# Optimization experiments

Hardware: AMD Instinct MI355X
Metric: run time of the kernel (lower is better)

The kernel has to match this reference:

```python
import jax, jax.numpy as jnp
import numpy as np

B, C, T, H, F, KS = 8, 512, 1024, 8, 2048, 3
K = C // H            # head channels = 64
ROPE_D = K // 2       # RoPE rotates half the head channels = 32
EPS = 1e-4


def setup_inputs() -> dict:
    key = jax.random.key(0)
    ks = jax.random.split(key, 12)
    s = 1.0 / np.sqrt(C)
    sf = 1.0 / np.sqrt(F)
    return {
        "x": jax.random.normal(ks[0], (B, C, T), jnp.float32),
        "x_mask": jnp.ones((B, 1, T), jnp.float32),
        "attn_mask": jnp.ones((B, 1, T, T), jnp.float32),
        "wq": jax.random.normal(ks[1], (C, C), jnp.float32) * s,
        "bq": jnp.zeros((C,), jnp.float32),
        "wk": jax.random.normal(ks[2], (C, C), jnp.float32) * s,
        "bk": jnp.zeros((C,), jnp.float32),
        "wv": jax.random.normal(ks[3], (C, C), jnp.float32) * s,
        "bv": jnp.zeros((C,), jnp.float32),
        "wo": jax.random.normal(ks[4], (C, C), jnp.float32) * s,
        "bo": jnp.zeros((C,), jnp.float32),
        "w1": jax.random.normal(ks[5], (F, C, KS), jnp.float32) * s,
        "b1": jnp.zeros((F,), jnp.float32),
        "w2": jax.random.normal(ks[6], (C, F, KS), jnp.float32) * sf,
        "b2": jnp.zeros((C,), jnp.float32),
        "g1": jnp.ones((C,), jnp.float32),
        "be1": jnp.zeros((C,), jnp.float32),
        "g2": jnp.ones((C,), jnp.float32),
        "be2": jnp.zeros((C,), jnp.float32),
    }


def _rope(x):
    # x: (B, H, T, K); rotate first ROPE_D channels, pass the rest through.
    t = x.shape[2]
    theta = 1.0 / (10000.0 ** (jnp.arange(0, ROPE_D, 2, dtype=jnp.float32) / ROPE_D))
    idx = jnp.arange(t, dtype=jnp.float32)[:, None] * theta[None, :]  # (T, d/2)
    idx2 = jnp.concatenate([idx, idx], axis=-1)                       # (T, d)
    cos, sin = jnp.cos(idx2), jnp.sin(idx2)                           # broadcast over B,H
    xr, xp = x[..., :ROPE_D], x[..., ROPE_D:]
    h = ROPE_D // 2
    neg = jnp.concatenate([-xr[..., h:], xr[..., :h]], axis=-1)
    return jnp.concatenate([xr * cos + neg * sin, xp], axis=-1)


def _ln(x, gamma, beta):
    # channel-wise LayerNorm over dim 1 of (B, C, T), eps=1e-4
    mean = jnp.mean(x, axis=1, keepdims=True)
    var = jnp.mean((x - mean) ** 2, axis=1, keepdims=True)
    xn = (x - mean) * jax.lax.rsqrt(var + EPS)
    return xn * gamma[None, :, None] + beta[None, :, None]


def _conv1d(x, w, b):
    # x: (B, Cin, T), w: (Cout, Cin, KS), 'same' padding (KS//2)
    y = jax.lax.conv_general_dilated(
        x, w, window_strides=(1,), padding=[(KS // 2, KS // 2)],
        dimension_numbers=("NCH", "OIH", "NCH"))
    return y + b[None, :, None]


def _forward(x, x_mask, attn_mask, wq, bq, wk, bk, wv, bv, wo, bo,
             w1, b1, w2, b2, g1, be1, g2, be2):
    x = x * x_mask
    # 1x1 conv projections == channel matmuls
    q = jnp.einsum("oc,bct->bot", wq, x) + bq[None, :, None]
    k = jnp.einsum("oc,bct->bot", wk, x) + bk[None, :, None]
    v = jnp.einsum("oc,bct->bot", wv, x) + bv[None, :, None]
    # (B, C, T) -> (B, H, T, K)
    def heads(a):
        return a.reshape(B, H, K, T).transpose(0, 1, 3, 2)
    q, k, v = heads(q), heads(k), heads(v)
    q = _rope(q)
    k = _rope(k)
    scores = jnp.einsum("bhtk,bhsk->bhts", q, k) / jnp.sqrt(jnp.float32(K))
    scores = jnp.where(attn_mask == 0, jnp.float32(-10000.0), scores)
    p = jax.nn.softmax(scores, axis=-1)
    o = jnp.einsum("bhts,bhsk->bhtk", p, v)              # (B,H,T,K)
    o = o.transpose(0, 1, 3, 2).reshape(B, C, T)
    y = jnp.einsum("oc,bct->bot", wo, o) + bo[None, :, None]
    x = _ln(x + y, g1, be1)
    # conv FFN
    h1 = jax.nn.relu(_conv1d(x * x_mask, w1, b1))
    y = _conv1d(h1 * x_mask, w2, b2) * x_mask
    x = _ln(x + y, g2, be2)
    return x


def reference(x, x_mask, attn_mask, wq, bq, wk, bk, wv, bv, wo, bo,
              w1, b1, w2, b2, g1, be1, g2, be2):
    return _forward(x, x_mask, attn_mask, wq, bq, wk, bk, wv, bv, wo, bo,
                    w1, b1, w2, b2, g1, be1, g2, be2)
```

## Files before the change

### kernel.cpp

```cpp
#include <hip/hip_runtime.h>

typedef unsigned short u16;
typedef __attribute__((ext_vector_type(4))) float floatx4;
typedef __attribute__((ext_vector_type(8))) __bf16 bf16x8;
typedef __attribute__((ext_vector_type(4))) unsigned short ushort4v;
typedef __attribute__((ext_vector_type(8))) unsigned short ushort8v;

#define DI __device__ __forceinline__


DI u16 f2bf(float f) {
  union { float f; unsigned u; } v; v.f = f;
  unsigned r = v.u + 0x7fffu + ((v.u >> 16) & 1u);
  return (u16)(r >> 16);
}
DI float bf2f(u16 h) {
  union { unsigned u; float f; } v; v.u = ((unsigned)h) << 16;
  return v.f;
}

#define GLDS(g, l) __builtin_amdgcn_global_load_lds( \
    (const __attribute__((address_space(1))) unsigned int*)(g), \
    (__attribute__((address_space(3))) unsigned int*)(l), 16, 0, 0)

__global__ __launch_bounds__(256) void k_fattn(
    const u16* __restrict__ qb, const u16* __restrict__ kb,
    const u16* __restrict__ vb, const unsigned* __restrict__ mb,
    u16* __restrict__ oT)
{
  __shared__ __align__(16) u16 Ps[4][32 * 64];
  const int tid  = threadIdx.x;
  const int wave = tid >> 6, lane = tid & 63;
  const int lr = lane & 15, kg = lane >> 4;
  const int qt = blockIdx.x, bh = blockIdx.y;
  const int bb = bh >> 3, hh = bh & 7;
  const int wq0 = qt * 128 + wave * 32;
  const float L2E = 1.44269504f;

  const u16* Qp = qb + (size_t)bh * 65536;
  const u16* Kp = kb + (size_t)bh * 65536;
  const u16* Vp = vb + (size_t)bh * 65536;
  u16* Pw = &Ps[wave][0];

  bf16x8 qf[2][2];
#pragma unroll
  for (int i = 0; i < 2; ++i)
#pragma unroll
    for (int h = 0; h < 2; ++h)
      qf[i][h] = *(const bf16x8*)&Qp[(wq0 + i * 16 + lr) * 64 + h * 32 + kg * 8];

  float m_b[2] = {-3.0e38f, -3.0e38f};
  float l_b[2] = {0.f, 0.f};
  floatx4 o_acc[2][4];
#pragma unroll
  for (int i = 0; i < 2; ++i)
#pragma unroll
    for (int j = 0; j < 4; ++j) o_acc[i][j] = (floatx4){0.f, 0.f, 0.f, 0.f};

  for (int s0 = 0; s0 < 1024; s0 += 64) {
    floatx4 sT[4][2];
#pragma unroll
    for (int a = 0; a < 4; ++a) {
      bf16x8 kf[2];
#pragma unroll
      for (int h = 0; h < 2; ++h)
        kf[h] = *(const bf16x8*)&Kp[(s0 + a * 16 + lr) * 64 + h * 32 + kg * 8];
      sT[a][0] = (floatx4){0.f, 0.f, 0.f, 0.f};
      sT[a][1] = (floatx4){0.f, 0.f, 0.f, 0.f};
#pragma unroll
      for (int b = 0; b < 2; ++b)
#pragma unroll
        for (int h = 0; h < 2; ++h)
          sT[a][b] = __builtin_amdgcn_mfma_f32_16x16x32_bf16(kf[h], qf[b][h], sT[a][b], 0, 0, 0);
    }
    float corr[2];
#pragma unroll
    for (int b = 0; b < 2; ++b) {
      const size_t rw = ((size_t)bb << 15) + ((size_t)(wq0 + b * 16 + lr) << 5) + (s0 >> 5);
      const unsigned w0 = mb[rw], w1 = mb[rw + 1];
      float mx = -3.0e38f;
#pragma unroll
      for (int a = 0; a < 4; ++a)
#pragma unroll
        for (int r = 0; r < 4; ++r) {
          const int sl = a * 16 + kg * 4 + r;
          float sv = sT[a][b][r] * 0.125f;
          const unsigned wsel = (sl & 32) ? w1 : w0;
          if (!((wsel >> (sl & 31)) & 1u)) sv = -10000.f;
          sT[a][b][r] = sv;
          mx = fmaxf(mx, sv);
        }
      mx = fmaxf(mx, __shfl_xor(mx, 16));
      mx = fmaxf(mx, __shfl_xor(mx, 32));
      const float mn = fmaxf(m_b[b], mx);
      corr[b] = exp2f((m_b[b] - mn) * L2E);
      m_b[b] = mn;
      float sum = 0.f;
#pragma unroll
      for (int a = 0; a < 4; ++a)
#pragma unroll
        for (int r = 0; r < 4; ++r) {
          const float p = exp2f((sT[a][b][r] - mn) * L2E);
          sT[a][b][r] = p;
          sum += p;
        }
      sum += __shfl_xor(sum, 16);
      sum += __shfl_xor(sum, 32);
      l_b[b] = l_b[b] * corr[b] + sum;
#pragma unroll
      for (int a = 0; a < 4; ++a)
#pragma unroll
        for (int r = 0; r < 4; ++r) {
          const int sl = a * 16 + kg * 4 + r;
          __bf16 hv = (__bf16)sT[a][b][r];
          Pw[(b * 16 + lr) * 64 + (sl ^ ((lr & 7) << 3))] = *(u16*)&hv;
        }
    }
#pragma unroll
    for (int i = 0; i < 2; ++i)
#pragma unroll
      for (int r = 0; r < 4; ++r) {
        const float cv = __shfl(corr[i], kg * 4 + r);
#pragma unroll
        for (int jd = 0; jd < 4; ++jd) o_acc[i][jd][r] *= cv;
      }
    asm volatile("s_waitcnt lgkmcnt(0)" ::: "memory");
    __builtin_amdgcn_sched_barrier(0);
    bf16x8 pa[2][2];
#pragma unroll
    for (int i = 0; i < 2; ++i)
#pragma unroll
      for (int h = 0; h < 2; ++h)
        pa[i][h] = *(const bf16x8*)&Pw[(i * 16 + lr) * 64 + (((h * 4 + kg) ^ (lr & 7)) << 3)];
#pragma unroll
    for (int jd = 0; jd < 4; ++jd) {
      bf16x8 vf[2];
#pragma unroll
      for (int h = 0; h < 2; ++h)
        vf[h] = *(const bf16x8*)&Vp[(jd * 16 + lr) * 1024 + s0 + h * 32 + kg * 8];
#pragma unroll
      for (int i = 0; i < 2; ++i)
#pragma unroll
        for (int h = 0; h < 2; ++h)
          o_acc[i][jd] = __builtin_amdgcn_mfma_f32_16x16x32_bf16(pa[i][h], vf[h], o_acc[i][jd], 0, 0, 0);
    }
  }
  float linv[2][4];
#pragma unroll
  for (int i = 0; i < 2; ++i)
#pragma unroll
    for (int r = 0; r < 4; ++r) linv[i][r] = 1.f / __shfl(l_b[i], kg * 4 + r);
#pragma unroll
  for (int i = 0; i < 2; ++i)
#pragma unroll
    for (int jd = 0; jd < 4; ++jd)
#pragma unroll
      for (int r = 0; r < 4; ++r) {
        const int t = wq0 + i * 16 + kg * 4 + r;
        const int c = hh * 64 + jd * 16 + lr;
        oT[((size_t)bb * 1024 + t) * 512 + c] = f2bf(o_acc[i][jd][r] * linv[i][r]);
      }
}

template<int MODE, int BN, int TAPK>
__global__ __launch_bounds__(256) void k_cgemm(
    const u16* __restrict__ A, int lda,
    const u16* __restrict__ Bsrc, int ldb,
    int K,
    u16* __restrict__ o0, u16* __restrict__ o1, u16* __restrict__ o2,
    const float* __restrict__ bias,
    const float* __restrict__ ctab, const float* __restrict__ stab,
    const float* __restrict__ msk)
{
  constexpr int BM = 128;
  constexpr int FN = BN / 32;
  __shared__ __align__(16) u16 As[2 * BM * 32];
  __shared__ __align__(16) u16 Bs[2 * BN * 32];

  const int tid  = threadIdx.x;
  const int wave = tid >> 6, lane = tid & 63;
  const int wm = wave >> 1, wn = wave & 1;
  const int lr = lane & 15, kg = lane >> 4;

  const int nwg = gridDim.x * gridDim.y;
  const int h0  = blockIdx.y * gridDim.x + blockIdx.x;
  const int cpx = nwg >> 3;
  const int tl  = (h0 & 7) * cpx + (h0 >> 3);
  const int bx  = tl % gridDim.x;
  const int by  = tl / gridDim.x;

  const int m0 = bx * BM, n0 = by * BN;
  const int koff = blockIdx.z * K;

  floatx4 acc[4][FN];
#pragma unroll
  for (int i = 0; i < 4; ++i)
#pragma unroll
    for (int j = 0; j < FN; ++j) acc[i][j] = (floatx4){0.f, 0.f, 0.f, 0.f};

  for (int k0 = 0; k0 < K; k0 += 64) {
#pragma unroll
    for (int h = 0; h < 2; ++h) {
      const int kglob = koff + k0 + h * 32;
#pragma unroll
      for (int ch = 0; ch < BM / 64; ++ch) {
        int idx = ch * 256 + tid;
        int row = idx >> 2, kk = (idx & 3) << 3;
        GLDS(A + (size_t)(m0 + row) * lda + (kglob + kk),
             &As[h * BM * 32 + idx * 8]);
      }
#pragma unroll
      for (int ch = 0; ch < BN / 64; ++ch) {
        int idx = ch * 256 + tid;
        int row = idx >> 2, kk = (idx & 3) << 3;
        const int bt = n0 + row;
        const u16* src;
        if constexpr (TAPK == 0) {
          src = Bsrc + (size_t)bt * ldb + (kglob + kk);
        } else {
          const int tap = kglob / TAPK, off2 = kglob - tap * TAPK;
          const int b = bt >> 10, t = bt & 1023;
          src = Bsrc + ((size_t)(b * 1026 + t + tap)) * TAPK + off2 + kk;
        }
        GLDS(src, &Bs[h * BN * 32 + idx * 8]);
      }
    }
    __syncthreads();
    bf16x8 af[2][4], bfr[2][FN];
#pragma unroll
    for (int h = 0; h < 2; ++h) {
#pragma unroll
      for (int i = 0; i < 4; ++i)
        af[h][i] = *(const bf16x8*)&As[(h * BM + wm * 64 + i * 16 + lr) * 32 + kg * 8];
#pragma unroll
      for (int j = 0; j < FN; ++j)
        bfr[h][j] = *(const bf16x8*)&Bs[(h * BN + wn * (BN / 2) + j * 16 + lr) * 32 + kg * 8];
    }
#pragma unroll
    for (int h = 0; h < 2; ++h)
#pragma unroll
      for (int i = 0; i < 4; ++i)
#pragma unroll
        for (int j = 0; j < FN; ++j)
          acc[i][j] = __builtin_amdgcn_mfma_f32_16x16x32_bf16(af[h][i], bfr[h][j], acc[i][j], 0, 0, 0);
    __syncthreads();
  }

  const int wrow0 = m0 + wm * 64;
  const int col0  = n0 + wn * (BN / 2);

  if constexpr (MODE == 0) {
    float v[4][FN][4];
#pragma unroll
    for (int i = 0; i < 4; ++i)
#pragma unroll
      for (int j = 0; j < FN; ++j)
#pragma unroll
        for (int r = 0; r < 4; ++r)
          v[i][j][r] = acc[i][j][r] + bias[wrow0 + i * 16 + kg * 4 + r];
    const int sec = wrow0 >> 9;
    const int hh  = (wrow0 & 511) >> 6;
    if (sec < 2) {
#pragma unroll
      for (int j = 0; j < FN; ++j) {
        const int t = (col0 + j * 16 + lr) & 1023;
#pragma unroll
        for (int r = 0; r < 4; ++r) {
          const int a = kg * 4 + r;
          const float cv = ctab[t * 16 + a], sv = stab[t * 16 + a];
          const float a0 = v[0][j][r], a1 = v[1][j][r];
          v[0][j][r] = a0 * cv - a1 * sv;
          v[1][j][r] = a1 * cv + a0 * sv;
        }
      }
      u16* dst = (sec == 0) ? o0 : o1;
#pragma unroll
      for (int i = 0; i < 4; ++i)
#pragma unroll
        for (int j = 0; j < FN; ++j) {
          const int bt = col0 + j * 16 + lr;
          const int b = bt >> 10, t = bt & 1023;
          ushort4v pk;
#pragma unroll
          for (int r = 0; r < 4; ++r) pk[r] = f2bf(v[i][j][r]);
          *(ushort4v*)&dst[(((size_t)b * 8 + hh) * 1024 + t) * 64 + i * 16 + kg * 4] = pk;
        }
    } else {
#pragma unroll
      for (int i = 0; i < 4; ++i)
#pragma unroll
        for (int j = 0; j < FN; ++j) {
          const int bt = col0 + j * 16 + lr;
          const int b = bt >> 10, t = bt & 1023;
#pragma unroll
          for (int r = 0; r < 4; ++r) {
            const int dk = i * 16 + kg * 4 + r;
            o2[(((size_t)b * 8 + hh) * 64 + dk) * 1024 + t] = f2bf(v[i][j][r]);
          }
        }
    }
  } else if constexpr (MODE == 3) {
#pragma unroll
    for (int i = 0; i < 4; ++i)
#pragma unroll
      for (int j = 0; j < FN; ++j) {
        const int bt = col0 + j * 16 + lr;
        const int c0 = wrow0 + i * 16 + kg * 4;
        ushort4v pk;
#pragma unroll
        for (int r = 0; r < 4; ++r) pk[r] = f2bf(acc[i][j][r] + bias[c0 + r]);
        *(ushort4v*)&o0[(size_t)bt * 512 + c0] = pk;
      }
  } else if constexpr (MODE == 4) {
#pragma unroll
    for (int i = 0; i < 4; ++i) {
      const int r0 = wrow0 + i * 16 + kg * 4;
#pragma unroll
      for (int j = 0; j < FN; ++j) {
        const int bt = col0 + j * 16 + lr;
        const int b = bt >> 10, t = bt & 1023;
        const float mv = msk[(size_t)b * 1024 + t];
        ushort4v pk;
#pragma unroll
        for (int r = 0; r < 4; ++r)
          pk[r] = f2bf(fmaxf(acc[i][j][r] + bias[r0 + r], 0.f) * mv);
        *(ushort4v*)&o0[((size_t)(b * 1026 + t + 1)) * 2048 + r0] = pk;
      }
    }
  } else {
    u16* dst = (blockIdx.z == 0) ? o0 : o1;
#pragma unroll
    for (int i = 0; i < 4; ++i)
#pragma unroll
      for (int j = 0; j < FN; ++j) {
        const int bt = col0 + j * 16 + lr;
        const int b = bt >> 10, t = bt & 1023;
        const int c0 = wrow0 + i * 16 + kg * 4;
        const float mv = msk[(size_t)b * 1024 + t];
        ushort4v pk;
#pragma unroll
        for (int r = 0; r < 4; ++r) {
          const float bv = (blockIdx.z == 0) ? bias[c0 + r] : 0.f;
          pk[r] = f2bf((acc[i][j][r] + bv) * mv);
        }
        *(ushort4v*)&dst[(size_t)bt * 512 + c0] = pk;
      }
  }
}

__global__ __launch_bounds__(256) void k_cvt(const float* __restrict__ in, u16* __restrict__ out, int n) {
  int i = blockIdx.x * 256 + threadIdx.x;
  if (i < n) out[i] = f2bf(in[i]);
}

__global__ __launch_bounds__(256) void k_repack_w1(const float* __restrict__ in, u16* __restrict__ out) {
  int i = blockIdx.x * 256 + threadIdx.x;
  int f = i / 1536, rem = i % 1536;
  int kk = rem >> 9, c = rem & 511;
  out[i] = f2bf(in[f * 1536 + c * 3 + kk]);
}

__global__ __launch_bounds__(256) void k_repack_w2(const float* __restrict__ in, u16* __restrict__ out) {
  int i = blockIdx.x * 256 + threadIdx.x;
  int c = i / 6144, rem = i % 6144;
  int kk = rem >> 11, f = rem & 2047;
  out[i] = f2bf(in[c * 6144 + f * 3 + kk]);
}

__global__ __launch_bounds__(256) void k_bias_concat(const float* __restrict__ bq, const float* __restrict__ bk,
                                                     const float* __restrict__ bv, float* __restrict__ out) {
  int i = blockIdx.x * 256 + threadIdx.x;
  if (i < 512) out[i] = bq[i];
  else if (i < 1024) out[i] = bk[i - 512];
  else if (i < 1536) out[i] = bv[i - 1024];
}

__global__ __launch_bounds__(256) void k_rope_tables(float* __restrict__ ct, float* __restrict__ st) {
  int i = blockIdx.x * 256 + threadIdx.x;
  int t = i >> 4, a = i & 15;
  float theta = powf(10000.f, -(float)a / 16.f);
  float ang = (float)t * theta;
  ct[i] = cosf(ang);
  st[i] = sinf(ang);
}

__global__ __launch_bounds__(256) void k_maskpack(const float* __restrict__ am, unsigned* __restrict__ mb) {
  int i = blockIdx.x * 256 + threadIdx.x;
  const float* src = am + (size_t)i * 32;
  unsigned w = 0;
#pragma unroll
  for (int q = 0; q < 32; ++q) w |= (src[q] != 0.f) ? (1u << q) : 0u;
  mb[i] = w;
}

__global__ __launch_bounds__(256) void k_zrows(u16* __restrict__ p, int R) {
  const int b = blockIdx.x >> 1;
  const size_t row = (blockIdx.x & 1) ? 1025 : 0;
  u16* r = p + ((size_t)b * 1026 + row) * R;
  for (int i = threadIdx.x; i < R; i += 256) r[i] = 0;
}

__global__ __launch_bounds__(256) void k_tcvt(const float* __restrict__ in, u16* __restrict__ out,
                                              const float* __restrict__ msk, int R, int TT) {
  __shared__ u16 tile[64][65];
  const int b = blockIdx.z;
  const int r0 = blockIdx.x * 64, t0 = blockIdx.y * 64;
  const int tx = threadIdx.x & 63, ty = threadIdx.x >> 6;
  const float mv = msk ? msk[(size_t)b * TT + t0 + tx] : 1.f;
  const float* ib = in + (size_t)b * R * TT;
#pragma unroll
  for (int rr = ty; rr < 64; rr += 4)
    tile[rr][tx] = f2bf(ib[(size_t)(r0 + rr) * TT + t0 + tx] * mv);
  __syncthreads();
  u16* ob = out + (size_t)b * TT * R;
#pragma unroll
  for (int tt = ty; tt < 64; tt += 4)
    ob[(size_t)(t0 + tt) * R + r0 + tx] = tile[tx][tt];
}

__global__ __launch_bounds__(256) void k_ln1(
    const u16* __restrict__ xbT, const u16* __restrict__ y1T,
    const float* __restrict__ xm, const float* __restrict__ g,
    const float* __restrict__ be, u16* __restrict__ x2T, u16* __restrict__ x2p)
{
  const int lane = threadIdx.x & 63, wv = threadIdx.x >> 6;
  const int row = blockIdx.x * 4 + wv;
  const int b = row >> 10, t = row & 1023;
  const size_t base = (size_t)row * 512 + lane * 8;
  ushort8v ux = *(const ushort8v*)&xbT[base];
  ushort8v uy = *(const ushort8v*)&y1T[base];
  float v[8];
  float sum = 0.f, ss = 0.f;
#pragma unroll
  for (int q = 0; q < 8; ++q) {
    v[q] = bf2f(ux[q]) + bf2f(uy[q]);
    sum += v[q]; ss += v[q] * v[q];
  }
#pragma unroll
  for (int o = 32; o; o >>= 1) { sum += __shfl_xor(sum, o); ss += __shfl_xor(ss, o); }
  const float mean = sum * (1.f / 512.f);
  const float var  = ss * (1.f / 512.f) - mean * mean;
  const float rs   = rsqrtf(var + 1e-4f);
  const float m    = xm[(size_t)b * 1024 + t];
  ushort8v on, om;
#pragma unroll
  for (int q = 0; q < 8; ++q) {
    const int c = lane * 8 + q;
    const float nv = (v[q] - mean) * rs * g[c] + be[c];
    on[q] = f2bf(nv);
    om[q] = f2bf(nv * m);
  }
  *(ushort8v*)&x2T[base] = on;
  *(ushort8v*)&x2p[((size_t)(b * 1026 + t + 1)) * 512 + lane * 8] = om;
}

__global__ __launch_bounds__(256) void k_ln2_stats(
    const u16* __restrict__ x2T, const u16* __restrict__ y2a,
    const u16* __restrict__ y2b, float2* __restrict__ mr)
{
  const int lane = threadIdx.x & 63, wv = threadIdx.x >> 6;
  const int row = blockIdx.x * 4 + wv;
  const size_t base = (size_t)row * 512 + lane * 8;
  ushort8v u0 = *(const ushort8v*)&x2T[base];
  ushort8v u1 = *(const ushort8v*)&y2a[base];
  ushort8v u2 = *(const ushort8v*)&y2b[base];
  float sum = 0.f, ss = 0.f;
#pragma unroll
  for (int q = 0; q < 8; ++q) {
    const float v = bf2f(u0[q]) + bf2f(u1[q]) + bf2f(u2[q]);
    sum += v; ss += v * v;
  }
#pragma unroll
  for (int o = 32; o; o >>= 1) { sum += __shfl_xor(sum, o); ss += __shfl_xor(ss, o); }
  if (lane == 0) {
    const float mean = sum * (1.f / 512.f);
    const float var  = ss * (1.f / 512.f) - mean * mean;
    mr[row] = (float2){mean, rsqrtf(var + 1e-4f)};
  }
}

__global__ __launch_bounds__(256) void k_ln2_write(
    const u16* __restrict__ x2T, const u16* __restrict__ y2a,
    const u16* __restrict__ y2b, const float2* __restrict__ mr,
    const float* __restrict__ g, const float* __restrict__ be,
    float* __restrict__ out)
{
  __shared__ float tile[64][65];
  const int cc0 = blockIdx.x * 64, t0 = blockIdx.y * 64, b = blockIdx.z;
  const int tid = threadIdx.x;
  const int c4 = (tid & 15) * 4;
  const int tr = tid >> 4;
  float g4[4], b4[4];
#pragma unroll
  for (int q = 0; q < 4; ++q) { g4[q] = g[cc0 + c4 + q]; b4[q] = be[cc0 + c4 + q]; }
#pragma unroll
  for (int it = 0; it < 4; ++it) {
    const int tt = tr + it * 16;
    const int row = b * 1024 + t0 + tt;
    const size_t base = (size_t)row * 512 + cc0 + c4;
    ushort4v u0 = *(const ushort4v*)&x2T[base];
    ushort4v u1 = *(const ushort4v*)&y2a[base];
    ushort4v u2 = *(const ushort4v*)&y2b[base];
    const float2 s = mr[row];
#pragma unroll
    for (int q = 0; q < 4; ++q) {
      const float v = bf2f(u0[q]) + bf2f(u1[q]) + bf2f(u2[q]);
      tile[tt][c4 + q] = (v - s.x) * s.y * g4[q] + b4[q];
    }
  }
  __syncthreads();
  const int tx = tid & 63, cg = tid >> 6;
#pragma unroll
  for (int c = cg; c < 64; c += 4)
    out[((size_t)b * 512 + cc0 + c) * 1024 + t0 + tx] = tile[tx][c];
}

extern "C" void kernel_launch(void* const* d_in, const int* in_sizes, int n_in,
                              void* d_out, int out_size, void* d_ws, size_t ws_size,
                              hipStream_t stream) {
  (void)in_sizes; (void)n_in; (void)out_size; (void)ws_size;
  const float* x   = (const float*)d_in[0];
  const float* xm  = (const float*)d_in[1];
  const float* am  = (const float*)d_in[2];
  const float* wq  = (const float*)d_in[3];
  const float* bq  = (const float*)d_in[4];
  const float* wk  = (const float*)d_in[5];
  const float* bk  = (const float*)d_in[6];
  const float* wv  = (const float*)d_in[7];
  const float* bv  = (const float*)d_in[8];
  const float* wo  = (const float*)d_in[9];
  const float* bo  = (const float*)d_in[10];
  const float* w1  = (const float*)d_in[11];
  const float* b1  = (const float*)d_in[12];
  const float* w2  = (const float*)d_in[13];
  const float* b2  = (const float*)d_in[14];
  const float* g1  = (const float*)d_in[15];
  const float* be1 = (const float*)d_in[16];
  const float* g2  = (const float*)d_in[17];
  const float* be2 = (const float*)d_in[18];
  float* out = (float*)d_out;

  char* ws = (char*)d_ws;
  size_t off = 0;
  auto alloc = [&](size_t bytes) { char* p = ws + off; off += (bytes + 255) & ~(size_t)255; return p; };

  u16*   wqkv = (u16*)  alloc((size_t)1536 * 512 * 2);
  u16*   wob  = (u16*)  alloc((size_t)512 * 512 * 2);
  u16*   w1p  = (u16*)  alloc((size_t)2048 * 1536 * 2);
  u16*   w2p  = (u16*)  alloc((size_t)512 * 6144 * 2);
  float* bqkv = (float*)alloc(1536 * 4);
  float* ctab = (float*)alloc(1024 * 16 * 4);
  float* stab = (float*)alloc(1024 * 16 * 4);
  unsigned* mbits = (unsigned*)alloc((size_t)8 * 1024 * 32 * 4);
  float2* mr  = (float2*)alloc((size_t)8192 * 8);
  u16*   x2T  = (u16*)  alloc((size_t)8 * 1024 * 512 * 2);
  u16*   x2p  = (u16*)  alloc((size_t)8 * 1026 * 512 * 2);
  u16*   h1p  = (u16*)  alloc((size_t)8 * 1026 * 2048 * 2);
  u16*   y1T  = (u16*)  alloc((size_t)8 * 1024 * 512 * 2);
  u16*   xbT  = (u16*)  alloc((size_t)8 * 1024 * 512 * 2);
  u16*   oT   = (u16*)  alloc((size_t)8 * 1024 * 512 * 2);
  u16*   qkv3 = (u16*)  alloc((size_t)3 * 8 * 8 * 1024 * 64 * 2);

  u16* qb   = qkv3;
  u16* kb   = qkv3 + (size_t)8 * 8 * 1024 * 64;
  u16* vb   = kb   + (size_t)8 * 8 * 1024 * 64;
  u16* y2aT = y1T;
  u16* y2bT = oT;

  dim3 blk(256);

  k_cvt<<<dim3(1024), blk, 0, stream>>>(wq, wqkv, 512 * 512);
  k_cvt<<<dim3(1024), blk, 0, stream>>>(wk, wqkv + 512 * 512, 512 * 512);
  k_cvt<<<dim3(1024), blk, 0, stream>>>(wv, wqkv + 2 * 512 * 512, 512 * 512);
  k_cvt<<<dim3(1024), blk, 0, stream>>>(wo, wob, 512 * 512);
  k_repack_w1<<<dim3(12288), blk, 0, stream>>>(w1, w1p);
  k_repack_w2<<<dim3(12288), blk, 0, stream>>>(w2, w2p);
  k_bias_concat<<<dim3(6), blk, 0, stream>>>(bq, bk, bv, bqkv);
  k_rope_tables<<<dim3(64), blk, 0, stream>>>(ctab, stab);
  k_maskpack<<<dim3(1024), blk, 0, stream>>>(am, mbits);
  k_zrows<<<dim3(16), blk, 0, stream>>>(x2p, 512);
  k_zrows<<<dim3(16), blk, 0, stream>>>(h1p, 2048);

  k_tcvt<<<dim3(8, 16, 8), blk, 0, stream>>>(x, xbT, xm, 512, 1024);

  k_cgemm<0, 128, 0><<<dim3(12, 64), blk, 0, stream>>>(
      wqkv, 512, xbT, 512, 512, qb, kb, vb, bqkv, ctab, stab, nullptr);

  k_fattn<<<dim3(8, 64), blk, 0, stream>>>(qb, kb, vb, mbits, oT);

  k_cgemm<3, 64, 0><<<dim3(4, 128), blk, 0, stream>>>(
      wob, 512, oT, 512, 512, y1T, nullptr, nullptr, bo, nullptr, nullptr, nullptr);

  k_ln1<<<dim3(2048), blk, 0, stream>>>(xbT, y1T, xm, g1, be1, x2T, x2p);

  k_cgemm<4, 128, 512><<<dim3(16, 64), blk, 0, stream>>>(
      w1p, 1536, x2p, 0, 1536, h1p, nullptr, nullptr, b1, nullptr, nullptr, xm);
  k_cgemm<5, 64, 2048><<<dim3(4, 128, 2), blk, 0, stream>>>(
      w2p, 6144, h1p, 0, 3072, y2aT, y2bT, nullptr, b2, nullptr, nullptr, xm);

  k_ln2_stats<<<dim3(2048), blk, 0, stream>>>(x2T, y2aT, y2bT, mr);
  k_ln2_write<<<dim3(8, 16, 8), blk, 0, stream>>>(x2T, y2aT, y2bT, mr, g2, be2, out);
}
```

Before: 332.3 us.

## Double-buffer GEMM LDS tiles, XOR-swizzle LDS layout, shrink BN for QKV/FFN1

The shared GEMM kernel now ping-pongs two LDS buffers, so the global-to-LDS async loads for the next K-slice are issued before the MFMAs on the current slice. That removes one barrier per iteration and hides load latency. Row-dependent XOR swizzling of the 8-element column chunks is meant to cut LDS bank conflicts on the fragment reads. The QKV and first-conv GEMMs also switch from a 128 to a 64 column tile with twice the grid, which adds occupancy and offsets the doubled LDS footprint at the cost of less operand reuse per block.

```diff
diff --git a/kernel.cpp b/kernel.cpp
--- a/kernel.cpp
+++ b/kernel.cpp
@@ -174,8 +174,8 @@
 {
   constexpr int BM = 128;
   constexpr int FN = BN / 32;
-  __shared__ __align__(16) u16 As[2 * BM * 32];
-  __shared__ __align__(16) u16 Bs[2 * BN * 32];
+  __shared__ __align__(16) u16 As[2][2 * BM * 32];
+  __shared__ __align__(16) u16 Bs[2][2 * BN * 32];
 
   const int tid  = threadIdx.x;
   const int wave = tid >> 6, lane = tid & 63;
@@ -192,27 +192,23 @@
   const int m0 = bx * BM, n0 = by * BN;
   const int koff = blockIdx.z * K;
 
-  floatx4 acc[4][FN];
-#pragma unroll
-  for (int i = 0; i < 4; ++i)
-#pragma unroll
-    for (int j = 0; j < FN; ++j) acc[i][j] = (floatx4){0.f, 0.f, 0.f, 0.f};
-
-  for (int k0 = 0; k0 < K; k0 += 64) {
+  auto stage = [&](int buf, int kbase) {
 #pragma unroll
     for (int h = 0; h < 2; ++h) {
-      const int kglob = koff + k0 + h * 32;
+      const int kglob = kbase + h * 32;
 #pragma unroll
       for (int ch = 0; ch < BM / 64; ++ch) {
-        int idx = ch * 256 + tid;
-        int row = idx >> 2, kk = (idx & 3) << 3;
+        const int idx = ch * 256 + tid;
+        const int row = idx >> 2;
+        const int kk = (((idx & 3) ^ ((row >> 1) & 3)) << 3);
         GLDS(A + (size_t)(m0 + row) * lda + (kglob + kk),
-             &As[h * BM * 32 + idx * 8]);
+             &As[buf][h * BM * 32 + idx * 8]);
       }
 #pragma unroll
       for (int ch = 0; ch < BN / 64; ++ch) {
-        int idx = ch * 256 + tid;
-        int row = idx >> 2, kk = (idx & 3) << 3;
+        const int idx = ch * 256 + tid;
+        const int row = idx >> 2;
+        const int kk = (((idx & 3) ^ ((row >> 1) & 3)) << 3);
         const int bt = n0 + row;
         const u16* src;
         if constexpr (TAPK == 0) {
@@ -222,19 +218,33 @@
           const int b = bt >> 10, t = bt & 1023;
           src = Bsrc + ((size_t)(b * 1026 + t + tap)) * TAPK + off2 + kk;
         }
-        GLDS(src, &Bs[h * BN * 32 + idx * 8]);
-      }
-    }
-    __syncthreads();
+        GLDS(src, &Bs[buf][h * BN * 32 + idx * 8]);
+      }
+    }
+  };
+
+  floatx4 acc[4][FN];
+#pragma unroll
+  for (int i = 0; i < 4; ++i)
+#pragma unroll
+    for (int j = 0; j < FN; ++j) acc[i][j] = (floatx4){0.f, 0.f, 0.f, 0.f};
+
+  const int csw = (kg ^ ((lr >> 1) & 3)) * 8;
+
+  stage(0, koff);
+  __syncthreads();
+  int cur = 0;
+  for (int k0 = 0; k0 < K; k0 += 64) {
+    if (k0 + 64 < K) stage(cur ^ 1, koff + k0 + 64);
     bf16x8 af[2][4], bfr[2][FN];
 #pragma unroll
     for (int h = 0; h < 2; ++h) {
 #pragma unroll
       for (int i = 0; i < 4; ++i)
-        af[h][i] = *(const bf16x8*)&As[(h * BM + wm * 64 + i * 16 + lr) * 32 + kg * 8];
+        af[h][i] = *(const bf16x8*)&As[cur][(h * BM + wm * 64 + i * 16 + lr) * 32 + csw];
 #pragma unroll
       for (int j = 0; j < FN; ++j)
-        bfr[h][j] = *(const bf16x8*)&Bs[(h * BN + wn * (BN / 2) + j * 16 + lr) * 32 + kg * 8];
+        bfr[h][j] = *(const bf16x8*)&Bs[cur][(h * BN + wn * (BN / 2) + j * 16 + lr) * 32 + csw];
     }
 #pragma unroll
     for (int h = 0; h < 2; ++h)
@@ -244,6 +254,7 @@
         for (int j = 0; j < FN; ++j)
           acc[i][j] = __builtin_amdgcn_mfma_f32_16x16x32_bf16(af[h][i], bfr[h][j], acc[i][j], 0, 0, 0);
     __syncthreads();
+    cur ^= 1;
   }
 
   const int wrow0 = m0 + wm * 64;
@@ -583,7 +594,7 @@
 
   k_tcvt<<<dim3(8, 16, 8), blk, 0, stream>>>(x, xbT, xm, 512, 1024);
 
-  k_cgemm<0, 128, 0><<<dim3(12, 64), blk, 0, stream>>>(
+  k_cgemm<0, 64, 0><<<dim3(12, 128), blk, 0, stream>>>(
       wqkv, 512, xbT, 512, 512, qb, kb, vb, bqkv, ctab, stab, nullptr);
 
   k_fattn<<<dim3(8, 64), blk, 0, stream>>>(qb, kb, vb, mbits, oT);
@@ -593,7 +604,7 @@
 
   k_ln1<<<dim3(2048), blk, 0, stream>>>(xbT, y1T, xm, g1, be1, x2T, x2p);
 
-  k_cgemm<4, 128, 512><<<dim3(16, 64), blk, 0, stream>>>(
+  k_cgemm<4, 64, 512><<<dim3(16, 128), blk, 0, stream>>>(
       w1p, 1536, x2p, 0, 1536, h1p, nullptr, nullptr, b1, nullptr, nullptr, xm);
   k_cgemm<5, 64, 2048><<<dim3(4, 128, 2), blk, 0, stream>>>(
       w2p, 6144, h1p, 0, 3072, y2aT, y2bT, nullptr, b2, nullptr, nullptr, xm);
```

Measured after the change: 349.5 us. +5.2%, slower.

## Halve attention query tile per wave, prefetch K/V, swizzle GEMM LDS

Applied to the files above, without the earlier changes.

The flash-attention kernel now handles 16 query rows per wave instead of 32 and launches twice as many blocks. It also loads all K and V fragments before their MFMA loops and raises wave priority around those loops, aiming for more parallelism and better latency hiding. In exchange, each K/V load is reused by half as many queries, so global/L2 traffic roughly doubles. Separately, the GEMM kernel XOR-swizzles the 16-byte column chunks in LDS on both the write and read side to reduce bank conflicts.

```diff
diff --git a/kernel.cpp b/kernel.cpp
--- a/kernel.cpp
+++ b/kernel.cpp
@@ -28,13 +28,13 @@
     const u16* __restrict__ vb, const unsigned* __restrict__ mb,
     u16* __restrict__ oT)
 {
-  __shared__ __align__(16) u16 Ps[4][32 * 64];
+  __shared__ __align__(16) u16 Ps[4][16 * 64];
   const int tid  = threadIdx.x;
   const int wave = tid >> 6, lane = tid & 63;
   const int lr = lane & 15, kg = lane >> 4;
   const int qt = blockIdx.x, bh = blockIdx.y;
   const int bb = bh >> 3, hh = bh & 7;
-  const int wq0 = qt * 128 + wave * 32;
+  const int wq0 = qt * 64 + wave * 16;
   const float L2E = 1.44269504f;
 
   const u16* Qp = qb + (size_t)bh * 65536;
@@ -42,124 +42,110 @@
   const u16* Vp = vb + (size_t)bh * 65536;
   u16* Pw = &Ps[wave][0];
 
-  bf16x8 qf[2][2];
-#pragma unroll
-  for (int i = 0; i < 2; ++i)
-#pragma unroll
-    for (int h = 0; h < 2; ++h)
-      qf[i][h] = *(const bf16x8*)&Qp[(wq0 + i * 16 + lr) * 64 + h * 32 + kg * 8];
-
-  float m_b[2] = {-3.0e38f, -3.0e38f};
-  float l_b[2] = {0.f, 0.f};
-  floatx4 o_acc[2][4];
-#pragma unroll
-  for (int i = 0; i < 2; ++i)
-#pragma unroll
-    for (int j = 0; j < 4; ++j) o_acc[i][j] = (floatx4){0.f, 0.f, 0.f, 0.f};
+  bf16x8 qf[2];
+#pragma unroll
+  for (int h = 0; h < 2; ++h)
+    qf[h] = *(const bf16x8*)&Qp[(wq0 + lr) * 64 + h * 32 + kg * 8];
+
+  float m_b = -3.0e38f;
+  float l_b = 0.f;
+  floatx4 o_acc[4];
+#pragma unroll
+  for (int j = 0; j < 4; ++j) o_acc[j] = (floatx4){0.f, 0.f, 0.f, 0.f};
 
   for (int s0 = 0; s0 < 1024; s0 += 64) {
-    floatx4 sT[4][2];
+    floatx4 sT[4];
+    bf16x8 kf[4][2];
+#pragma unroll
+    for (int a = 0; a < 4; ++a)
+#pragma unroll
+      for (int h = 0; h < 2; ++h)
+        kf[a][h] = *(const bf16x8*)&Kp[(s0 + a * 16 + lr) * 64 + h * 32 + kg * 8];
+    __builtin_amdgcn_s_setprio(1);
 #pragma unroll
     for (int a = 0; a < 4; ++a) {
-      bf16x8 kf[2];
+      sT[a] = (floatx4){0.f, 0.f, 0.f, 0.f};
 #pragma unroll
       for (int h = 0; h < 2; ++h)
-        kf[h] = *(const bf16x8*)&Kp[(s0 + a * 16 + lr) * 64 + h * 32 + kg * 8];
-      sT[a][0] = (floatx4){0.f, 0.f, 0.f, 0.f};
-      sT[a][1] = (floatx4){0.f, 0.f, 0.f, 0.f};
-#pragma unroll
-      for (int b = 0; b < 2; ++b)
-#pragma unroll
-        for (int h = 0; h < 2; ++h)
-          sT[a][b] = __builtin_amdgcn_mfma_f32_16x16x32_bf16(kf[h], qf[b][h], sT[a][b], 0, 0, 0);
-    }
-    float corr[2];
-#pragma unroll
-    for (int b = 0; b < 2; ++b) {
-      const size_t rw = ((size_t)bb << 15) + ((size_t)(wq0 + b * 16 + lr) << 5) + (s0 >> 5);
-      const unsigned w0 = mb[rw], w1 = mb[rw + 1];
-      float mx = -3.0e38f;
-#pragma unroll
-      for (int a = 0; a < 4; ++a)
-#pragma unroll
-        for (int r = 0; r < 4; ++r) {
-          const int sl = a * 16 + kg * 4 + r;
-          float sv = sT[a][b][r] * 0.125f;
-          const unsigned wsel = (sl & 32) ? w1 : w0;
-          if (!((wsel >> (sl & 31)) & 1u)) sv = -10000.f;
-          sT[a][b][r] = sv;
-          mx = fmaxf(mx, sv);
-        }
-      mx = fmaxf(mx, __shfl_xor(mx, 16));
-      mx = fmaxf(mx, __shfl_xor(mx, 32));
-      const float mn = fmaxf(m_b[b], mx);
-      corr[b] = exp2f((m_b[b] - mn) * L2E);
-      m_b[b] = mn;
-      float sum = 0.f;
-#pragma unroll
-      for (int a = 0; a < 4; ++a)
-#pragma unroll
-        for (int r = 0; r < 4; ++r) {
-          const float p = exp2f((sT[a][b][r] - mn) * L2E);
-          sT[a][b][r] = p;
-          sum += p;
-        }
-      sum += __shfl_xor(sum, 16);
-      sum += __shfl_xor(sum, 32);
-      l_b[b] = l_b[b] * corr[b] + sum;
-#pragma unroll
-      for (int a = 0; a < 4; ++a)
-#pragma unroll
-        for (int r = 0; r < 4; ++r) {
-          const int sl = a * 16 + kg * 4 + r;
-          __bf16 hv = (__bf16)sT[a][b][r];
-          Pw[(b * 16 + lr) * 64 + (sl ^ ((lr & 7) << 3))] = *(u16*)&hv;
-        }
-    }
-#pragma unroll
-    for (int i = 0; i < 2; ++i)
+        sT[a] = __builtin_amdgcn_mfma_f32_16x16x32_bf16(kf[a][h], qf[h], sT[a], 0, 0, 0);
+    }
+    __builtin_amdgcn_s_setprio(0);
+    const size_t rw = ((size_t)bb << 15) + ((size_t)(wq0 + lr) << 5) + (s0 >> 5);
+    const unsigned w0 = mb[rw], w1 = mb[rw + 1];
+    float mx = -3.0e38f;
+#pragma unroll
+    for (int a = 0; a < 4; ++a)
 #pragma unroll
       for (int r = 0; r < 4; ++r) {
-        const float cv = __shfl(corr[i], kg * 4 + r);
-#pragma unroll
-        for (int jd = 0; jd < 4; ++jd) o_acc[i][jd][r] *= cv;
-      }
+        const int sl = a * 16 + kg * 4 + r;
+        float sv = sT[a][r] * 0.125f;
+        const unsigned wsel = (sl & 32) ? w1 : w0;
+        if (!((wsel >> (sl & 31)) & 1u)) sv = -10000.f;
+        sT[a][r] = sv;
+        mx = fmaxf(mx, sv);
+      }
+    mx = fmaxf(mx, __shfl_xor(mx, 16));
+    mx = fmaxf(mx, __shfl_xor(mx, 32));
+    const float mn = fmaxf(m_b, mx);
+    const float corr = exp2f((m_b - mn) * L2E);
+    m_b = mn;
+    float sum = 0.f;
+#pragma unroll
+    for (int a = 0; a < 4; ++a)
+#pragma unroll
+      for (int r = 0; r < 4; ++r) {
+        const float p = exp2f((sT[a][r] - mn) * L2E);
+        sT[a][r] = p;
+        sum += p;
+      }
+    sum += __shfl_xor(sum, 16);
+    sum += __shfl_xor(sum, 32);
+    l_b = l_b * corr + sum;
+#pragma unroll
+    for (int a = 0; a < 4; ++a)
+#pragma unroll
+      for (int r = 0; r < 4; ++r) {
+        const int sl = a * 16 + kg * 4 + r;
+        __bf16 hv = (__bf16)sT[a][r];
+        Pw[lr * 64 + (sl ^ ((lr & 7) << 3))] = *(u16*)&hv;
+      }
+#pragma unroll
+    for (int r = 0; r < 4; ++r) {
+      const float cv = __shfl(corr, kg * 4 + r);
+#pragma unroll
+      for (int jd = 0; jd < 4; ++jd) o_acc[jd][r] *= cv;
+    }
     asm volatile("s_waitcnt lgkmcnt(0)" ::: "memory");
     __builtin_amdgcn_sched_barrier(0);
-    bf16x8 pa[2][2];
-#pragma unroll
-    for (int i = 0; i < 2; ++i)
+    bf16x8 pa[2];
+#pragma unroll
+    for (int h = 0; h < 2; ++h)
+      pa[h] = *(const bf16x8*)&Pw[lr * 64 + (((h * 4 + kg) ^ (lr & 7)) << 3)];
+    bf16x8 vf[4][2];
+#pragma unroll
+    for (int jd = 0; jd < 4; ++jd)
 #pragma unroll
       for (int h = 0; h < 2; ++h)
-        pa[i][h] = *(const bf16x8*)&Pw[(i * 16 + lr) * 64 + (((h * 4 + kg) ^ (lr & 7)) << 3)];
-#pragma unroll
-    for (int jd = 0; jd < 4; ++jd) {
-      bf16x8 vf[2];
+        vf[jd][h] = *(const bf16x8*)&Vp[(jd * 16 + lr) * 1024 + s0 + h * 32 + kg * 8];
+    __builtin_amdgcn_s_setprio(1);
+#pragma unroll
+    for (int jd = 0; jd < 4; ++jd)
 #pragma unroll
       for (int h = 0; h < 2; ++h)
-        vf[h] = *(const bf16x8*)&Vp[(jd * 16 + lr) * 1024 + s0 + h * 32 + kg * 8];
-#pragma unroll
-      for (int i = 0; i < 2; ++i)
-#pragma unroll
-        for (int h = 0; h < 2; ++h)
-          o_acc[i][jd] = __builtin_amdgcn_mfma_f32_16x16x32_bf16(pa[i][h], vf[h], o_acc[i][jd], 0, 0, 0);
-    }
-  }
-  float linv[2][4];
-#pragma unroll
-  for (int i = 0; i < 2; ++i)
-#pragma unroll
-    for (int r = 0; r < 4; ++r) linv[i][r] = 1.f / __shfl(l_b[i], kg * 4 + r);
-#pragma unroll
-  for (int i = 0; i < 2; ++i)
-#pragma unroll
-    for (int jd = 0; jd < 4; ++jd)
-#pragma unroll
-      for (int r = 0; r < 4; ++r) {
-        const int t = wq0 + i * 16 + kg * 4 + r;
-        const int c = hh * 64 + jd * 16 + lr;
-        oT[((size_t)bb * 1024 + t) * 512 + c] = f2bf(o_acc[i][jd][r] * linv[i][r]);
-      }
+        o_acc[jd] = __builtin_amdgcn_mfma_f32_16x16x32_bf16(pa[h], vf[jd][h], o_acc[jd], 0, 0, 0);
+    __builtin_amdgcn_s_setprio(0);
+  }
+  float linv[4];
+#pragma unroll
+  for (int r = 0; r < 4; ++r) linv[r] = 1.f / __shfl(l_b, kg * 4 + r);
+#pragma unroll
+  for (int jd = 0; jd < 4; ++jd)
+#pragma unroll
+    for (int r = 0; r < 4; ++r) {
+      const int t = wq0 + kg * 4 + r;
+      const int c = hh * 64 + jd * 16 + lr;
+      oT[((size_t)bb * 1024 + t) * 512 + c] = f2bf(o_acc[jd][r] * linv[r]);
+    }
 }
 
 template<int MODE, int BN, int TAPK>
@@ -198,21 +184,25 @@
 #pragma unroll
     for (int j = 0; j < FN; ++j) acc[i][j] = (floatx4){0.f, 0.f, 0.f, 0.f};
 
+  const int csw = (kg ^ ((lr >> 1) & 3)) * 8;
+
   for (int k0 = 0; k0 < K; k0 += 64) {
 #pragma unroll
     for (int h = 0; h < 2; ++h) {
       const int kglob = koff + k0 + h * 32;
 #pragma unroll
       for (int ch = 0; ch < BM / 64; ++ch) {
-        int idx = ch * 256 + tid;
-        int row = idx >> 2, kk = (idx & 3) << 3;
+        const int idx = ch * 256 + tid;
+        const int row = idx >> 2;
+        const int kk = (((idx & 3) ^ ((row >> 1) & 3)) << 3);
         GLDS(A + (size_t)(m0 + row) * lda + (kglob + kk),
              &As[h * BM * 32 + idx * 8]);
       }
 #pragma unroll
       for (int ch = 0; ch < BN / 64; ++ch) {
-        int idx = ch * 256 + tid;
-        int row = idx >> 2, kk = (idx & 3) << 3;
+        const int idx = ch * 256 + tid;
+        const int row = idx >> 2;
+        const int kk = (((idx & 3) ^ ((row >> 1) & 3)) << 3);
         const int bt = n0 + row;
         const u16* src;
         if constexpr (TAPK == 0) {
@@ -231,10 +221,10 @@
     for (int h = 0; h < 2; ++h) {
 #pragma unroll
       for (int i = 0; i < 4; ++i)
-        af[h][i] = *(const bf16x8*)&As[(h * BM + wm * 64 + i * 16 + lr) * 32 + kg * 8];
+        af[h][i] = *(const bf16x8*)&As[(h * BM + wm * 64 + i * 16 + lr) * 32 + csw];
 #pragma unroll
       for (int j = 0; j < FN; ++j)
-        bfr[h][j] = *(const bf16x8*)&Bs[(h * BN + wn * (BN / 2) + j * 16 + lr) * 32 + kg * 8];
+        bfr[h][j] = *(const bf16x8*)&Bs[(h * BN + wn * (BN / 2) + j * 16 + lr) * 32 + csw];
     }
 #pragma unroll
     for (int h = 0; h < 2; ++h)
@@ -586,7 +576,7 @@
   k_cgemm<0, 128, 0><<<dim3(12, 64), blk, 0, stream>>>(
       wqkv, 512, xbT, 512, 512, qb, kb, vb, bqkv, ctab, stab, nullptr);
 
-  k_fattn<<<dim3(8, 64), blk, 0, stream>>>(qb, kb, vb, mbits, oT);
+  k_fattn<<<dim3(16, 64), blk, 0, stream>>>(qb, kb, vb, mbits, oT);
 
   k_cgemm<3, 64, 0><<<dim3(4, 128), blk, 0, stream>>>(
       wob, 512, oT, 512, 512, y1T, nullptr, nullptr, bo, nullptr, nullptr, nullptr);
```

New measurement: 401.1 us. +20.7%, slower.

## Prefetch K/V tiles into registers in attention; swizzle GEMM LDS layout

Applied to the files above, without the earlier changes.

The flash-attention kernel now loads the next iteration's K and V fragments into registers while computing the current tile. It also fully unrolls the key loop, raises wave priority around the MFMA blocks, and sets a two-blocks-per-CU launch bound. The GEMM kernel applies an XOR swizzle to the k-chunk position in the LDS tiles, on both the global-to-LDS writes and the fragment reads, to reduce bank conflicts. The register double-buffering adds VGPR pressure, which could conflict with the occupancy hint or cause spills.

```diff
diff --git a/kernel.cpp b/kernel.cpp
--- a/kernel.cpp
+++ b/kernel.cpp
@@ -23,7 +23,7 @@
     (const __attribute__((address_space(1))) unsigned int*)(g), \
     (__attribute__((address_space(3))) unsigned int*)(l), 16, 0, 0)
 
-__global__ __launch_bounds__(256) void k_fattn(
+__global__ __launch_bounds__(256, 2) void k_fattn(
     const u16* __restrict__ qb, const u16* __restrict__ kb,
     const u16* __restrict__ vb, const unsigned* __restrict__ mb,
     u16* __restrict__ oT)
@@ -57,22 +57,41 @@
 #pragma unroll
     for (int j = 0; j < 4; ++j) o_acc[i][j] = (floatx4){0.f, 0.f, 0.f, 0.f};
 
-  for (int s0 = 0; s0 < 1024; s0 += 64) {
+  bf16x8 kf[4][2], vf[4][2], kfn[4][2], vfn[4][2];
+#pragma unroll
+  for (int a = 0; a < 4; ++a)
+#pragma unroll
+    for (int h = 0; h < 2; ++h) {
+      kf[a][h] = *(const bf16x8*)&Kp[(a * 16 + lr) * 64 + h * 32 + kg * 8];
+      vf[a][h] = *(const bf16x8*)&Vp[(a * 16 + lr) * 1024 + h * 32 + kg * 8];
+    }
+
+#pragma unroll
+  for (int it = 0; it < 16; ++it) {
+    const int s0 = it * 64;
+    if (it < 15) {
+      const int sn = s0 + 64;
+#pragma unroll
+      for (int a = 0; a < 4; ++a)
+#pragma unroll
+        for (int h = 0; h < 2; ++h) {
+          kfn[a][h] = *(const bf16x8*)&Kp[(sn + a * 16 + lr) * 64 + h * 32 + kg * 8];
+          vfn[a][h] = *(const bf16x8*)&Vp[(a * 16 + lr) * 1024 + sn + h * 32 + kg * 8];
+        }
+    }
     floatx4 sT[4][2];
+    __builtin_amdgcn_s_setprio(1);
 #pragma unroll
     for (int a = 0; a < 4; ++a) {
-      bf16x8 kf[2];
-#pragma unroll
-      for (int h = 0; h < 2; ++h)
-        kf[h] = *(const bf16x8*)&Kp[(s0 + a * 16 + lr) * 64 + h * 32 + kg * 8];
       sT[a][0] = (floatx4){0.f, 0.f, 0.f, 0.f};
       sT[a][1] = (floatx4){0.f, 0.f, 0.f, 0.f};
 #pragma unroll
       for (int b = 0; b < 2; ++b)
 #pragma unroll
         for (int h = 0; h < 2; ++h)
-          sT[a][b] = __builtin_amdgcn_mfma_f32_16x16x32_bf16(kf[h], qf[b][h], sT[a][b], 0, 0, 0);
-    }
+          sT[a][b] = __builtin_amdgcn_mfma_f32_16x16x32_bf16(kf[a][h], qf[b][h], sT[a][b], 0, 0, 0);
+    }
+    __builtin_amdgcn_s_setprio(0);
     float corr[2];
 #pragma unroll
     for (int b = 0; b < 2; ++b) {
@@ -132,17 +151,23 @@
 #pragma unroll
       for (int h = 0; h < 2; ++h)
         pa[i][h] = *(const bf16x8*)&Pw[(i * 16 + lr) * 64 + (((h * 4 + kg) ^ (lr & 7)) << 3)];
-#pragma unroll
-    for (int jd = 0; jd < 4; ++jd) {
-      bf16x8 vf[2];
-#pragma unroll
-      for (int h = 0; h < 2; ++h)
-        vf[h] = *(const bf16x8*)&Vp[(jd * 16 + lr) * 1024 + s0 + h * 32 + kg * 8];
+    __builtin_amdgcn_s_setprio(1);
+#pragma unroll
+    for (int jd = 0; jd < 4; ++jd)
 #pragma unroll
       for (int i = 0; i < 2; ++i)
 #pragma unroll
         for (int h = 0; h < 2; ++h)
-          o_acc[i][jd] = __builtin_amdgcn_mfma_f32_16x16x32_bf16(pa[i][h], vf[h], o_acc[i][jd], 0, 0, 0);
+          o_acc[i][jd] = __builtin_amdgcn_mfma_f32_16x16x32_bf16(pa[i][h], vf[jd][h], o_acc[i][jd], 0, 0, 0);
+    __builtin_amdgcn_s_setprio(0);
+    if (it < 15) {
+#pragma unroll
+      for (int a = 0; a < 4; ++a)
+#pragma unroll
+        for (int h = 0; h < 2; ++h) {
+          kf[a][h] = kfn[a][h];
+          vf[a][h] = vfn[a][h];
+        }
     }
   }
   float linv[2][4];
@@ -198,21 +223,25 @@
 #pragma unroll
     for (int j = 0; j < FN; ++j) acc[i][j] = (floatx4){0.f, 0.f, 0.f, 0.f};
 
+  const int csw = (kg ^ ((lr >> 1) & 3)) * 8;
+
   for (int k0 = 0; k0 < K; k0 += 64) {
 #pragma unroll
     for (int h = 0; h < 2; ++h) {
       const int kglob = koff + k0 + h * 32;
 #pragma unroll
       for (int ch = 0; ch < BM / 64; ++ch) {
-        int idx = ch * 256 + tid;
-        int row = idx >> 2, kk = (idx & 3) << 3;
+        const int idx = ch * 256 + tid;
+        const int row = idx >> 2;
+        const int kk = (((idx & 3) ^ ((row >> 1) & 3)) << 3);
         GLDS(A + (size_t)(m0 + row) * lda + (kglob + kk),
              &As[h * BM * 32 + idx * 8]);
       }
 #pragma unroll
       for (int ch = 0; ch < BN / 64; ++ch) {
-        int idx = ch * 256 + tid;
-        int row = idx >> 2, kk = (idx & 3) << 3;
+        const int idx = ch * 256 + tid;
+        const int row = idx >> 2;
+        const int kk = (((idx & 3) ^ ((row >> 1) & 3)) << 3);
         const int bt = n0 + row;
         const u16* src;
         if constexpr (TAPK == 0) {
@@ -231,10 +260,10 @@
     for (int h = 0; h < 2; ++h) {
 #pragma unroll
       for (int i = 0; i < 4; ++i)
-        af[h][i] = *(const bf16x8*)&As[(h * BM + wm * 64 + i * 16 + lr) * 32 + kg * 8];
+        af[h][i] = *(const bf16x8*)&As[(h * BM + wm * 64 + i * 16 + lr) * 32 + csw];
 #pragma unroll
       for (int j = 0; j < FN; ++j)
-        bfr[h][j] = *(const bf16x8*)&Bs[(h * BN + wn * (BN / 2) + j * 16 + lr) * 32 + kg * 8];
+        bfr[h][j] = *(const bf16x8*)&Bs[(h * BN + wn * (BN / 2) + j * 16 + lr) * 32 + csw];
     }
 #pragma unroll
     for (int h = 0; h < 2; ++h)
```

New measurement: 345.4 us. +3.9%, slower.
